# Kernel optimization log

Hardware: AMD Instinct MI355X
Metric: run time of the kernel (lower is better)

Reference implementation:

```python
import jax, jax.numpy as jnp
import numpy as np


def setup_inputs() -> dict:
    key = jax.random.key(0)
    b, t, e, h = 4, 2048, 768, 8
    ks = jax.random.split(key, 5)
    s_in = 1.0 / np.sqrt(e)
    s_out = 1.0 / np.sqrt(h * e)
    return {
        "x": jax.random.normal(ks[0], (b, t, e), dtype=jnp.float32),
        "Wq": jax.random.normal(ks[1], (e, h * e), dtype=jnp.float32) * s_in,
        "Wk": jax.random.normal(ks[2], (e, h * e), dtype=jnp.float32) * s_in,
        "Wv": jax.random.normal(ks[3], (e, h * e), dtype=jnp.float32) * s_in,
        "Wu": jax.random.normal(ks[4], (h * e, e), dtype=jnp.float32) * s_out,
        "bu": jnp.zeros((e,), dtype=jnp.float32),
    }


def reference(x, Wq, Wk, Wv, Wu, bu):
    # SelfAttentionWide: each head uses the FULL embedding dim e.
    b, t, e = x.shape
    h = Wq.shape[1] // e
    scale = e ** 0.25  # scale q and k each by e^(1/4) -> scores / sqrt(e)
    q = (x @ Wq).reshape(b, t, h, e) / scale
    k = (x @ Wk).reshape(b, t, h, e) / scale
    v = (x @ Wv).reshape(b, t, h, e)
    # full attention matrix [b, h, t, t] (no mask: mask=False)
    dot = jnp.einsum('bthe,bshe->bhts', q, k)
    att = jax.nn.softmax(dot, axis=-1)
    out = jnp.einsum('bhts,bshe->bthe', att, v).reshape(b, t, h * e)
    return out @ Wu + bu
```

## Files before the change

### kernel.cpp

```cpp
#include <hip/hip_runtime.h>
#include <hip/hip_bf16.h>
#include <cmath>

typedef __bf16 bf16;
typedef bf16 bf16x8 __attribute__((ext_vector_type(8)));
typedef bf16 bf16x4 __attribute__((ext_vector_type(4)));
typedef float f32x4 __attribute__((ext_vector_type(4)));

#define GLD_LDS16(g, l)                                                        \
    __builtin_amdgcn_global_load_lds(                                          \
        (__attribute__((address_space(1))) void*)(g),                          \
        (__attribute__((address_space(3))) void*)(l), 16, 0, 0)

__global__ __launch_bounds__(256) void convert_f32_bf16_k(
    const float* __restrict__ in, bf16* __restrict__ out, long n4)
{
    long i = (long)blockIdx.x * 256 + threadIdx.x;
    if (i < n4) {
        float4 v = reinterpret_cast<const float4*>(in)[i];
        bf16x4 o = { (bf16)v.x, (bf16)v.y, (bf16)v.z, (bf16)v.w };
        reinterpret_cast<bf16x4*>(out)[i] = o;
    }
}

__global__ __launch_bounds__(256) void transpose_f32_bf16_k(
    const float* __restrict__ in, bf16* __restrict__ out, int R, int C, float scale)
{
    __shared__ float tile[32][33];
    const int c = threadIdx.x & 31, r0 = threadIdx.x >> 5;
    const int ib = blockIdx.y * 32, ob = blockIdx.x * 32;
#pragma unroll
    for (int rr = 0; rr < 32; rr += 8)
        tile[r0 + rr][c] = in[(long)(ib + r0 + rr) * C + ob + c];
    __syncthreads();
#pragma unroll
    for (int rr = 0; rr < 32; rr += 8)
        out[(long)(ob + r0 + rr) * R + ib + c] = (bf16)(tile[c][r0 + rr] * scale);
}

__global__ __launch_bounds__(256) void transpose_bf16_k(
    const bf16* __restrict__ in, bf16* __restrict__ out, int R, int C, long inZ, long outZ)
{
    __shared__ bf16 tile[32][33];
    const long zi = (long)blockIdx.z * inZ, zo = (long)blockIdx.z * outZ;
    const int c = threadIdx.x & 31, r0 = threadIdx.x >> 5;
    const int ib = blockIdx.y * 32, ob = blockIdx.x * 32;
#pragma unroll
    for (int rr = 0; rr < 32; rr += 8)
        tile[r0 + rr][c] = in[zi + (long)(ib + r0 + rr) * C + ob + c];
    __syncthreads();
#pragma unroll
    for (int rr = 0; rr < 32; rr += 8)
        out[zo + (long)(ob + r0 + rr) * R + ib + c] = tile[c][r0 + rr];
}

__global__ __launch_bounds__(256) void reduce_bias_k(
    const float* __restrict__ part, const float* __restrict__ bias,
    float* __restrict__ out, int nChunks, long chunkElems, long n4)
{
    long i = (long)blockIdx.x * 256 + threadIdx.x;
    if (i >= n4) return;
    float4 s = reinterpret_cast<const float4*>(part)[i];
    for (int z = 1; z < nChunks; z++) {
        float4 v = reinterpret_cast<const float4*>(part + (long)z * chunkElems)[i];
        s.x += v.x; s.y += v.y; s.z += v.z; s.w += v.w;
    }
    const float4 bv = *reinterpret_cast<const float4*>(bias + ((i % 192) << 2));
    s.x += bv.x; s.y += bv.y; s.z += bv.z; s.w += bv.w;
    reinterpret_cast<float4*>(out)[i] = s;
}

template<int OUT_MODE>
__global__ __launch_bounds__(256, 2) void gemm_bt_k(
    const bf16* __restrict__ A, const bf16* __restrict__ B, void* __restrict__ Cv,
    int K, int lda, int ldb, long aZ, long bZ, long cZ,
    int Mb, long S1, int Nb, long S2, long rowStride,
    const float* __restrict__ bias, float* __restrict__ rowsum, long rsZ)
{
    __shared__ __align__(16) bf16 lA[128 * 64];
    __shared__ __align__(16) bf16 lB[128 * 64];
    const int tid = threadIdx.x;
    const int z = blockIdx.z;
    const int mBase = blockIdx.y * 128;
    const int nBase = blockIdx.x * 128;
    A += (long)z * aZ;
    B += (long)z * bZ;
    const long cbase = (long)z * cZ
        + (long)(mBase / Mb) * S1 + (long)(mBase % Mb) * rowStride
        + (long)(nBase / Nb) * S2 + (nBase % Nb);
    const int w = tid >> 6, l = tid & 63;
    const int wr = (w >> 1) * 64, wc = (w & 1) * 64;

    f32x4 acc[4][4];
#pragma unroll
    for (int i = 0; i < 4; i++)
#pragma unroll
        for (int j = 0; j < 4; j++)
            acc[i][j] = f32x4{0.f, 0.f, 0.f, 0.f};

    const int srow = tid >> 3;
    const int scol = (tid & 7) * 8;
    const bf16* ga = A + (long)(mBase + srow) * lda + scol;
    const bf16* gb = B + (long)(nBase + srow) * ldb + scol;
    char* lAb = reinterpret_cast<char*>(lA);
    char* lBb = reinterpret_cast<char*>(lB);
    const int ldsW = (tid & 192) * 16;

    const int aOff = (wr + (l & 15)) * 64 + (l >> 4) * 8;
    const int bOff = (wc + (l & 15)) * 64 + (l >> 4) * 8;

    for (int k0 = 0; k0 < K; k0 += 64) {
#pragma unroll
        for (int i = 0; i < 4; i++) {
            GLD_LDS16(ga + (long)i * 32 * lda + k0, lAb + i * 4096 + ldsW);
            GLD_LDS16(gb + (long)i * 32 * ldb + k0, lBb + i * 4096 + ldsW);
        }
        __syncthreads();
#pragma unroll
        for (int kk = 0; kk < 64; kk += 32) {
            bf16x8 af[4], bfr[4];
#pragma unroll
            for (int i = 0; i < 4; i++)
                af[i] = *reinterpret_cast<const bf16x8*>(lAb + (aOff + i * 1024 + kk) * 2);
#pragma unroll
            for (int j = 0; j < 4; j++)
                bfr[j] = *reinterpret_cast<const bf16x8*>(lBb + (bOff + j * 1024 + kk) * 2);
#pragma unroll
            for (int i = 0; i < 4; i++)
#pragma unroll
                for (int j = 0; j < 4; j++)
                    acc[i][j] = __builtin_amdgcn_mfma_f32_16x16x32_bf16(af[i], bfr[j], acc[i][j], 0, 0, 0);
        }
        __syncthreads();
    }

    const int lcol = l & 15;
    const int lrow = (l >> 4) * 4;

    if (OUT_MODE == 3) {
#pragma unroll
        for (int i = 0; i < 4; i++)
#pragma unroll
            for (int j = 0; j < 4; j++)
#pragma unroll
                for (int r = 0; r < 4; r++)
                    acc[i][j][r] = __expf(acc[i][j][r]);
#pragma unroll
        for (int i = 0; i < 4; i++)
#pragma unroll
            for (int r = 0; r < 4; r++) {
                float p = acc[i][0][r] + acc[i][1][r] + acc[i][2][r] + acc[i][3][r];
                p += __shfl_xor(p, 1);
                p += __shfl_xor(p, 2);
                p += __shfl_xor(p, 4);
                p += __shfl_xor(p, 8);
                if ((l & 15) == 0)
                    atomicAdd(&rowsum[(long)z * rsZ + mBase + wr + i * 16 + lrow + r], p);
            }
        bf16* C = reinterpret_cast<bf16*>(Cv);
#pragma unroll
        for (int i = 0; i < 4; i++)
#pragma unroll
            for (int j = 0; j < 4; j++)
#pragma unroll
                for (int r = 0; r < 4; r++)
                    C[cbase + (long)(wr + i * 16 + lrow + r) * rowStride + wc + j * 16 + lcol]
                        = (bf16)acc[i][j][r];
    } else if (OUT_MODE == 4) {
        bf16* C = reinterpret_cast<bf16*>(Cv);
#pragma unroll
        for (int i = 0; i < 4; i++)
#pragma unroll
            for (int r = 0; r < 4; r++) {
                const float inv = 1.0f / rowsum[(long)z * rsZ + mBase + wr + i * 16 + lrow + r];
#pragma unroll
                for (int j = 0; j < 4; j++)
                    C[cbase + (long)(wr + i * 16 + lrow + r) * rowStride + wc + j * 16 + lcol]
                        = (bf16)(acc[i][j][r] * inv);
            }
    } else if (OUT_MODE == 1) {
        bf16* C = reinterpret_cast<bf16*>(Cv);
#pragma unroll
        for (int i = 0; i < 4; i++)
#pragma unroll
            for (int j = 0; j < 4; j++)
#pragma unroll
                for (int r = 0; r < 4; r++)
                    C[cbase + (long)(wr + i * 16 + lrow + r) * rowStride + wc + j * 16 + lcol]
                        = (bf16)acc[i][j][r];
    } else {
        float* C = reinterpret_cast<float*>(Cv);
        float bv[4] = {0.f, 0.f, 0.f, 0.f};
        if (OUT_MODE == 2) {
#pragma unroll
            for (int j = 0; j < 4; j++)
                bv[j] = bias[nBase + wc + j * 16 + lcol];
        }
#pragma unroll
        for (int i = 0; i < 4; i++)
#pragma unroll
            for (int j = 0; j < 4; j++)
#pragma unroll
                for (int r = 0; r < 4; r++)
                    C[cbase + (long)(wr + i * 16 + lrow + r) * rowStride + wc + j * 16 + lcol]
                        = acc[i][j][r] + bv[j];
    }
}

extern "C" void kernel_launch(void* const* d_in, const int* in_sizes, int n_in,
                              void* d_out, int out_size, void* d_ws, size_t ws_size,
                              hipStream_t stream)
{
    const float* x  = (const float*)d_in[0];
    const float* Wq = (const float*)d_in[1];
    const float* Wk = (const float*)d_in[2];
    const float* Wv = (const float*)d_in[3];
    const float* Wu = (const float*)d_in[4];
    const float* bu = (const float*)d_in[5];
    float* out = (float*)d_out;

    constexpr int Bb = 4, T = 2048, E = 768, H = 8, HE = 6144, BT = 8192;
    constexpr int QKVN = 3 * HE;
    const int BIG = 1 << 30;

    char* ws = (char*)d_ws;
    size_t off = 0;
    auto alloc = [&](size_t bytes) { size_t o = off; off += (bytes + 255) & ~(size_t)255; return o; };
    bf16* Wqkvt  = (bf16*)(ws + alloc((size_t)QKVN * E * 2));
    bf16* Wut    = (bf16*)(ws + alloc((size_t)E * HE * 2));
    bf16* xb     = (bf16*)(ws + alloc((size_t)BT * E * 2));
    bf16* QKVb   = (bf16*)(ws + alloc((size_t)24 * T * E * 2));
    bf16* Vt     = (bf16*)(ws + alloc((size_t)H * E * T * 2));
    bf16* Ob     = (bf16*)(ws + alloc((size_t)T * HE * 2));
    float* rowsum= (float*)(ws + alloc((size_t)Bb * H * T * 4));
    size_t ebOff = off;
    int hc = 8;
    while (hc > 1 && ebOff + (size_t)hc * T * T * 2 > ws_size) hc >>= 1;
    bf16* Eb = (bf16*)(ws + ebOff);
    float* Cpart = (float*)(ws + ebOff);
    size_t avail = ws_size > ebOff ? ws_size - ebOff : (size_t)hc * T * T * 2;
    int nCh = 8;
    while (nCh > 1 && (size_t)nCh * T * E * 4 > avail) nCh >>= 1;
    const int Kc = HE / nCh;

    const float qs = 1.0f / powf((float)E, 0.25f);

    convert_f32_bf16_k<<<dim3((BT * E / 4) / 256), dim3(256), 0, stream>>>(x, xb, (long)BT * E / 4);
    transpose_f32_bf16_k<<<dim3(HE / 32, E / 32), dim3(256), 0, stream>>>(Wq, Wqkvt, E, HE, qs);
    transpose_f32_bf16_k<<<dim3(HE / 32, E / 32), dim3(256), 0, stream>>>(Wk, Wqkvt + (size_t)HE * E, E, HE, qs);
    transpose_f32_bf16_k<<<dim3(HE / 32, E / 32), dim3(256), 0, stream>>>(Wv, Wqkvt + (size_t)2 * HE * E, E, HE, 1.0f);
    transpose_f32_bf16_k<<<dim3(E / 32, HE / 32), dim3(256), 0, stream>>>(Wu, Wut, HE, E, 1.0f);
    hipMemsetAsync(rowsum, 0, (size_t)Bb * H * T * 4, stream);

    for (int b = 0; b < Bb; b++) {
        float* rs = rowsum + (long)b * H * T;
        gemm_bt_k<1><<<dim3(QKVN / 128, T / 128, 1), dim3(256), 0, stream>>>(
            xb + (long)b * T * E, Wqkvt, QKVb, E, E, E, 0, 0, 0,
            BIG, 0, E, (long)T * E, E, nullptr, nullptr, 0);

        transpose_bf16_k<<<dim3(E / 32, T / 32, H), dim3(256), 0, stream>>>(
            QKVb + (size_t)16 * T * E, Vt, T, E, (long)T * E, (long)E * T);

        for (int h0 = 0; h0 < H; h0 += hc) {
            gemm_bt_k<3><<<dim3(T / 128, T / 128, hc), dim3(256), 0, stream>>>(
                QKVb + (long)h0 * T * E, QKVb + (long)(8 + h0) * T * E, Eb,
                E, E, E, (long)T * E, (long)T * E, (long)T * T,
                BIG, 0, BIG, 0, T, nullptr, rs + (long)h0 * T, T);
            gemm_bt_k<4><<<dim3(E / 128, T / 128, hc), dim3(256), 0, stream>>>(
                Eb, Vt + (long)h0 * E * T, Ob + (long)h0 * E,
                T, T, T, (long)T * T, (long)E * T, (long)E,
                BIG, 0, BIG, 0, HE, nullptr, rs + (long)h0 * T, T);
        }

        gemm_bt_k<5><<<dim3(E / 128, T / 128, nCh), dim3(256), 0, stream>>>(
            Ob, Wut, Cpart, Kc, HE, HE, (long)Kc, (long)Kc, (long)T * E,
            BIG, 0, BIG, 0, E, nullptr, nullptr, 0);
        reduce_bias_k<<<dim3((T * E / 4 + 255) / 256), dim3(256), 0, stream>>>(
            Cpart, bu, out + (long)b * T * E, nCh, (long)T * E, (long)T * E / 4);
    }
}
```

Baseline: 1.347 ms.

## Add 256x256-tile 512-thread GEMM with 4-slot LDS pipeline for QKV and attention

Adds a new GEMM kernel using 256x256 output tiles and 8 waves. It streams K in 32-wide half-stages into four LDS slots via direct global-to-LDS loads, with an XOR swizzle to avoid bank conflicts, explicit vmcnt waits and barriers, and raised MFMA priority. The QKV projection, exp-scores and PV GEMMs switch to this kernel to get more reuse per tile and overlap loads with MFMA. The trade-off is 128KB of LDS per block and fewer blocks for the small E dimension: the PV GEMM has only three column tiles.

```diff
diff --git a/kernel.cpp b/kernel.cpp
--- a/kernel.cpp
+++ b/kernel.cpp
@@ -11,6 +11,10 @@
     __builtin_amdgcn_global_load_lds(                                          \
         (__attribute__((address_space(1))) void*)(g),                          \
         (__attribute__((address_space(3))) void*)(l), 16, 0, 0)
+
+#define SBAR asm volatile("s_barrier" ::: "memory")
+#define VMC4 asm volatile("s_waitcnt vmcnt(4)" ::: "memory")
+#define VMC0 asm volatile("s_waitcnt vmcnt(0)" ::: "memory")
 
 __global__ __launch_bounds__(256) void convert_f32_bf16_k(
     const float* __restrict__ in, bf16* __restrict__ out, long n4)
@@ -68,6 +72,203 @@
     const float4 bv = *reinterpret_cast<const float4*>(bias + ((i % 192) << 2));
     s.x += bv.x; s.y += bv.y; s.z += bv.z; s.w += bv.w;
     reinterpret_cast<float4*>(out)[i] = s;
+}
+
+template<int OUT_MODE>
+__global__ __launch_bounds__(512, 2) void gemm256_k(
+    const bf16* __restrict__ A, const bf16* __restrict__ B, void* __restrict__ Cv,
+    int K, int lda, int ldb, long aZ, long bZ, long cZ,
+    int Mb, long S1, int Nb, long S2, long rowStride,
+    float* __restrict__ rowsum, long rsZ)
+{
+    __shared__ __align__(16) char ldsmem[131072];
+    char* ldsb = ldsmem;
+    const int tid = threadIdx.x;
+    const int z = blockIdx.z;
+    const int mBase = blockIdx.y * 256;
+    const int nBase = blockIdx.x * 256;
+    A += (long)z * aZ + (long)mBase * lda;
+    B += (long)z * bZ + (long)nBase * ldb;
+    const long cbase = (long)z * cZ
+        + (long)(mBase / Mb) * S1 + (long)(mBase % Mb) * rowStride
+        + (long)(nBase / Nb) * S2 + (nBase % Nb);
+    const int w = tid >> 6, l = tid & 63;
+    const int wm = w >> 2, wn = w & 3;
+    const int lr = l & 15, lk = l >> 4;
+
+    f32x4 acc[8][4];
+#pragma unroll
+    for (int i = 0; i < 8; i++)
+#pragma unroll
+        for (int j = 0; j < 4; j++)
+            acc[i][j] = f32x4{0.f, 0.f, 0.f, 0.f};
+
+    const int c0 = (w << 7) + l, c1 = c0 + 64;
+    const int L0 = c0 ^ ((c0 >> 3) & 3), L1 = c1 ^ ((c1 >> 3) & 3);
+    const bf16* gA0 = A + (long)(L0 >> 2) * lda + (L0 & 3) * 8;
+    const bf16* gA1 = A + (long)(L1 >> 2) * lda + (L1 & 3) * 8;
+    const bf16* gB0 = B + (long)(L0 >> 2) * ldb + (L0 & 3) * 8;
+    const bf16* gB1 = B + (long)(L1 >> 2) * ldb + (L1 & 3) * 8;
+    const int dstw = w << 11;
+
+    int offA[8], offB[4];
+#pragma unroll
+    for (int mf = 0; mf < 8; mf++) {
+        int row = (wm << 7) + (mf << 4) + lr;
+        offA[mf] = ((row << 6) + (lk << 4)) ^ (((row >> 1) & 3) << 4);
+    }
+#pragma unroll
+    for (int nf = 0; nf < 4; nf++) {
+        int row = (wn << 6) + (nf << 4) + lr;
+        offB[nf] = ((row << 6) + (lk << 4)) ^ (((row >> 1) & 3) << 4);
+    }
+
+    bf16x8 av0, av1, av2, av3, bv0, bv1, bv2, bv3;
+
+#define STAGE_A(slot, kofs) do {                                               \
+    GLD_LDS16(gA0 + (kofs), ldsb + (slot) * 32768 + dstw);                     \
+    GLD_LDS16(gA1 + (kofs), ldsb + (slot) * 32768 + dstw + 1024); } while (0)
+#define STAGE_B(slot, kofs) do {                                               \
+    GLD_LDS16(gB0 + (kofs), ldsb + (slot) * 32768 + 16384 + dstw);             \
+    GLD_LDS16(gB1 + (kofs), ldsb + (slot) * 32768 + 16384 + dstw + 1024); } while (0)
+#define LD_A(s, mg) do {                                                       \
+    const char* _p = ldsb + (s) * 32768;                                       \
+    av0 = *(const bf16x8*)(_p + offA[(mg) * 4 + 0]);                           \
+    av1 = *(const bf16x8*)(_p + offA[(mg) * 4 + 1]);                           \
+    av2 = *(const bf16x8*)(_p + offA[(mg) * 4 + 2]);                           \
+    av3 = *(const bf16x8*)(_p + offA[(mg) * 4 + 3]); } while (0)
+#define LD_B(s) do {                                                           \
+    const char* _p = ldsb + (s) * 32768 + 16384;                               \
+    bv0 = *(const bf16x8*)(_p + offB[0]);                                      \
+    bv1 = *(const bf16x8*)(_p + offB[1]);                                      \
+    bv2 = *(const bf16x8*)(_p + offB[2]);                                      \
+    bv3 = *(const bf16x8*)(_p + offB[3]); } while (0)
+#define MFMA16(mg) do {                                                        \
+    acc[(mg)*4+0][0] = __builtin_amdgcn_mfma_f32_16x16x32_bf16(av0, bv0, acc[(mg)*4+0][0], 0, 0, 0); \
+    acc[(mg)*4+0][1] = __builtin_amdgcn_mfma_f32_16x16x32_bf16(av0, bv1, acc[(mg)*4+0][1], 0, 0, 0); \
+    acc[(mg)*4+0][2] = __builtin_amdgcn_mfma_f32_16x16x32_bf16(av0, bv2, acc[(mg)*4+0][2], 0, 0, 0); \
+    acc[(mg)*4+0][3] = __builtin_amdgcn_mfma_f32_16x16x32_bf16(av0, bv3, acc[(mg)*4+0][3], 0, 0, 0); \
+    acc[(mg)*4+1][0] = __builtin_amdgcn_mfma_f32_16x16x32_bf16(av1, bv0, acc[(mg)*4+1][0], 0, 0, 0); \
+    acc[(mg)*4+1][1] = __builtin_amdgcn_mfma_f32_16x16x32_bf16(av1, bv1, acc[(mg)*4+1][1], 0, 0, 0); \
+    acc[(mg)*4+1][2] = __builtin_amdgcn_mfma_f32_16x16x32_bf16(av1, bv2, acc[(mg)*4+1][2], 0, 0, 0); \
+    acc[(mg)*4+1][3] = __builtin_amdgcn_mfma_f32_16x16x32_bf16(av1, bv3, acc[(mg)*4+1][3], 0, 0, 0); \
+    acc[(mg)*4+2][0] = __builtin_amdgcn_mfma_f32_16x16x32_bf16(av2, bv0, acc[(mg)*4+2][0], 0, 0, 0); \
+    acc[(mg)*4+2][1] = __builtin_amdgcn_mfma_f32_16x16x32_bf16(av2, bv1, acc[(mg)*4+2][1], 0, 0, 0); \
+    acc[(mg)*4+2][2] = __builtin_amdgcn_mfma_f32_16x16x32_bf16(av2, bv2, acc[(mg)*4+2][2], 0, 0, 0); \
+    acc[(mg)*4+2][3] = __builtin_amdgcn_mfma_f32_16x16x32_bf16(av2, bv3, acc[(mg)*4+2][3], 0, 0, 0); \
+    acc[(mg)*4+3][0] = __builtin_amdgcn_mfma_f32_16x16x32_bf16(av3, bv0, acc[(mg)*4+3][0], 0, 0, 0); \
+    acc[(mg)*4+3][1] = __builtin_amdgcn_mfma_f32_16x16x32_bf16(av3, bv1, acc[(mg)*4+3][1], 0, 0, 0); \
+    acc[(mg)*4+3][2] = __builtin_amdgcn_mfma_f32_16x16x32_bf16(av3, bv2, acc[(mg)*4+3][2], 0, 0, 0); \
+    acc[(mg)*4+3][3] = __builtin_amdgcn_mfma_f32_16x16x32_bf16(av3, bv3, acc[(mg)*4+3][3], 0, 0, 0); } while (0)
+
+    const int nt = K >> 6;
+
+    STAGE_A(0, 0); STAGE_B(0, 0);
+    STAGE_A(1, 32); STAGE_B(1, 32);
+    VMC4; SBAR;
+
+    for (int t = 0; t < nt - 1; ++t) {
+        const int s0 = (t & 1) << 1, s1 = s0 | 1;
+        const int q0 = s0 ^ 2, q1 = s1 ^ 2;
+        const int kof = (t + 1) << 6;
+        LD_A(s0, 0); LD_B(s0);
+        STAGE_A(q0, kof);
+        __builtin_amdgcn_sched_barrier(0);
+        __builtin_amdgcn_s_setprio(1); MFMA16(0); __builtin_amdgcn_s_setprio(0);
+        SBAR;
+        LD_A(s0, 1);
+        STAGE_B(q0, kof);
+        __builtin_amdgcn_sched_barrier(0);
+        __builtin_amdgcn_s_setprio(1); MFMA16(1); __builtin_amdgcn_s_setprio(0);
+        VMC4;
+        SBAR;
+        LD_A(s1, 0); LD_B(s1);
+        STAGE_A(q1, kof + 32);
+        __builtin_amdgcn_sched_barrier(0);
+        __builtin_amdgcn_s_setprio(1); MFMA16(0); __builtin_amdgcn_s_setprio(0);
+        SBAR;
+        LD_A(s1, 1);
+        STAGE_B(q1, kof + 32);
+        __builtin_amdgcn_sched_barrier(0);
+        __builtin_amdgcn_s_setprio(1); MFMA16(1); __builtin_amdgcn_s_setprio(0);
+        VMC4;
+        SBAR;
+    }
+    {
+        const int s0 = ((nt - 1) & 1) << 1, s1 = s0 | 1;
+        LD_A(s0, 0); LD_B(s0);
+        __builtin_amdgcn_s_setprio(1); MFMA16(0); __builtin_amdgcn_s_setprio(0);
+        SBAR;
+        LD_A(s0, 1);
+        __builtin_amdgcn_s_setprio(1); MFMA16(1); __builtin_amdgcn_s_setprio(0);
+        VMC0;
+        SBAR;
+        LD_A(s1, 0); LD_B(s1);
+        __builtin_amdgcn_s_setprio(1); MFMA16(0); __builtin_amdgcn_s_setprio(0);
+        LD_A(s1, 1);
+        MFMA16(1);
+    }
+
+    const int rbase = (wm << 7) + (lk << 2);
+    const int colw = (wn << 6) + lr;
+
+    if (OUT_MODE == 3) {
+#pragma unroll
+        for (int mf = 0; mf < 8; mf++)
+#pragma unroll
+            for (int nf = 0; nf < 4; nf++)
+#pragma unroll
+                for (int r = 0; r < 4; r++)
+                    acc[mf][nf][r] = __expf(acc[mf][nf][r]);
+#pragma unroll
+        for (int mf = 0; mf < 8; mf++)
+#pragma unroll
+            for (int r = 0; r < 4; r++) {
+                float p = acc[mf][0][r] + acc[mf][1][r] + acc[mf][2][r] + acc[mf][3][r];
+                p += __shfl_xor(p, 1);
+                p += __shfl_xor(p, 2);
+                p += __shfl_xor(p, 4);
+                p += __shfl_xor(p, 8);
+                if (lr == 0)
+                    atomicAdd(&rowsum[(long)z * rsZ + mBase + rbase + mf * 16 + r], p);
+            }
+        bf16* C = reinterpret_cast<bf16*>(Cv);
+#pragma unroll
+        for (int mf = 0; mf < 8; mf++)
+#pragma unroll
+            for (int nf = 0; nf < 4; nf++)
+#pragma unroll
+                for (int r = 0; r < 4; r++)
+                    C[cbase + (long)(rbase + mf * 16 + r) * rowStride + colw + nf * 16]
+                        = (bf16)acc[mf][nf][r];
+    } else if (OUT_MODE == 4) {
+        bf16* C = reinterpret_cast<bf16*>(Cv);
+#pragma unroll
+        for (int mf = 0; mf < 8; mf++)
+#pragma unroll
+            for (int r = 0; r < 4; r++) {
+                const float inv = 1.0f / rowsum[(long)z * rsZ + mBase + rbase + mf * 16 + r];
+#pragma unroll
+                for (int nf = 0; nf < 4; nf++)
+                    C[cbase + (long)(rbase + mf * 16 + r) * rowStride + colw + nf * 16]
+                        = (bf16)(acc[mf][nf][r] * inv);
+            }
+    } else {
+        bf16* C = reinterpret_cast<bf16*>(Cv);
+#pragma unroll
+        for (int mf = 0; mf < 8; mf++)
+#pragma unroll
+            for (int nf = 0; nf < 4; nf++)
+#pragma unroll
+                for (int r = 0; r < 4; r++)
+                    C[cbase + (long)(rbase + mf * 16 + r) * rowStride + colw + nf * 16]
+                        = (bf16)acc[mf][nf][r];
+    }
+#undef STAGE_A
+#undef STAGE_B
+#undef LD_A
+#undef LD_B
+#undef MFMA16
 }
 
 template<int OUT_MODE>
@@ -136,75 +337,15 @@
 
     const int lcol = l & 15;
     const int lrow = (l >> 4) * 4;
-
-    if (OUT_MODE == 3) {
-#pragma unroll
-        for (int i = 0; i < 4; i++)
-#pragma unroll
-            for (int j = 0; j < 4; j++)
-#pragma unroll
-                for (int r = 0; r < 4; r++)
-                    acc[i][j][r] = __expf(acc[i][j][r]);
-#pragma unroll
-        for (int i = 0; i < 4; i++)
-#pragma unroll
-            for (int r = 0; r < 4; r++) {
-                float p = acc[i][0][r] + acc[i][1][r] + acc[i][2][r] + acc[i][3][r];
-                p += __shfl_xor(p, 1);
-                p += __shfl_xor(p, 2);
-                p += __shfl_xor(p, 4);
-                p += __shfl_xor(p, 8);
-                if ((l & 15) == 0)
-                    atomicAdd(&rowsum[(long)z * rsZ + mBase + wr + i * 16 + lrow + r], p);
-            }
-        bf16* C = reinterpret_cast<bf16*>(Cv);
-#pragma unroll
-        for (int i = 0; i < 4; i++)
-#pragma unroll
-            for (int j = 0; j < 4; j++)
-#pragma unroll
-                for (int r = 0; r < 4; r++)
-                    C[cbase + (long)(wr + i * 16 + lrow + r) * rowStride + wc + j * 16 + lcol]
-                        = (bf16)acc[i][j][r];
-    } else if (OUT_MODE == 4) {
-        bf16* C = reinterpret_cast<bf16*>(Cv);
-#pragma unroll
-        for (int i = 0; i < 4; i++)
-#pragma unroll
-            for (int r = 0; r < 4; r++) {
-                const float inv = 1.0f / rowsum[(long)z * rsZ + mBase + wr + i * 16 + lrow + r];
-#pragma unroll
-                for (int j = 0; j < 4; j++)
-                    C[cbase + (long)(wr + i * 16 + lrow + r) * rowStride + wc + j * 16 + lcol]
-                        = (bf16)(acc[i][j][r] * inv);
-            }
-    } else if (OUT_MODE == 1) {
-        bf16* C = reinterpret_cast<bf16*>(Cv);
-#pragma unroll
-        for (int i = 0; i < 4; i++)
-#pragma unroll
-            for (int j = 0; j < 4; j++)
-#pragma unroll
-                for (int r = 0; r < 4; r++)
-                    C[cbase + (long)(wr + i * 16 + lrow + r) * rowStride + wc + j * 16 + lcol]
-                        = (bf16)acc[i][j][r];
-    } else {
-        float* C = reinterpret_cast<float*>(Cv);
-        float bv[4] = {0.f, 0.f, 0.f, 0.f};
-        if (OUT_MODE == 2) {
-#pragma unroll
-            for (int j = 0; j < 4; j++)
-                bv[j] = bias[nBase + wc + j * 16 + lcol];
-        }
-#pragma unroll
-        for (int i = 0; i < 4; i++)
-#pragma unroll
-            for (int j = 0; j < 4; j++)
-#pragma unroll
-                for (int r = 0; r < 4; r++)
-                    C[cbase + (long)(wr + i * 16 + lrow + r) * rowStride + wc + j * 16 + lcol]
-                        = acc[i][j][r] + bv[j];
-    }
+    float* C = reinterpret_cast<float*>(Cv);
+#pragma unroll
+    for (int i = 0; i < 4; i++)
+#pragma unroll
+        for (int j = 0; j < 4; j++)
+#pragma unroll
+            for (int r = 0; r < 4; r++)
+                C[cbase + (long)(wr + i * 16 + lrow + r) * rowStride + wc + j * 16 + lcol]
+                    = acc[i][j][r];
 }
 
 extern "C" void kernel_launch(void* const* d_in, const int* in_sizes, int n_in,
@@ -254,22 +395,22 @@
 
     for (int b = 0; b < Bb; b++) {
         float* rs = rowsum + (long)b * H * T;
-        gemm_bt_k<1><<<dim3(QKVN / 128, T / 128, 1), dim3(256), 0, stream>>>(
+        gemm256_k<1><<<dim3(QKVN / 256, T / 256, 1), dim3(512), 0, stream>>>(
             xb + (long)b * T * E, Wqkvt, QKVb, E, E, E, 0, 0, 0,
-            BIG, 0, E, (long)T * E, E, nullptr, nullptr, 0);
+            BIG, 0, E, (long)T * E, E, nullptr, 0);
 
         transpose_bf16_k<<<dim3(E / 32, T / 32, H), dim3(256), 0, stream>>>(
             QKVb + (size_t)16 * T * E, Vt, T, E, (long)T * E, (long)E * T);
 
         for (int h0 = 0; h0 < H; h0 += hc) {
-            gemm_bt_k<3><<<dim3(T / 128, T / 128, hc), dim3(256), 0, stream>>>(
+            gemm256_k<3><<<dim3(T / 256, T / 256, hc), dim3(512), 0, stream>>>(
                 QKVb + (long)h0 * T * E, QKVb + (long)(8 + h0) * T * E, Eb,
                 E, E, E, (long)T * E, (long)T * E, (long)T * T,
-                BIG, 0, BIG, 0, T, nullptr, rs + (long)h0 * T, T);
-            gemm_bt_k<4><<<dim3(E / 128, T / 128, hc), dim3(256), 0, stream>>>(
+                BIG, 0, BIG, 0, T, rs + (long)h0 * T, T);
+            gemm256_k<4><<<dim3(E / 256, T / 256, hc), dim3(512), 0, stream>>>(
                 Eb, Vt + (long)h0 * E * T, Ob + (long)h0 * E,
                 T, T, T, (long)T * T, (long)E * T, (long)E,
-                BIG, 0, BIG, 0, HE, nullptr, rs + (long)h0 * T, T);
+                BIG, 0, BIG, 0, HE, rs + (long)h0 * T, T);
         }
 
         gemm_bt_k<5><<<dim3(E / 128, T / 128, nCh), dim3(256), 0, stream>>>(
```

Result: faster. 1.195 ms (-11.3%).
